# Optimization experiments

Measured on AMD Instinct MI355X. Metric: run time of the kernel, lower is better.

Reference implementation:

```python
import jax, jax.numpy as jnp
import numpy as np

NEG_INF = -1.0e9  # masked_fill value in the original


def gaussian_prior(n_heads, len_q, len_k, dtype=jnp.float32):
    """Per-head lower-triangular Gaussian positional bias.

    gm[h, i, j] = exp(-(j - i)^2 / (2 * sigma_h^2)) for i >= j, else 0.
    The buggy source never passes sigma_hs; we use sigma_h = h + 1 as a
    deterministic per-head bandwidth (wider Gaussians for later heads).
    """
    i = jnp.arange(len_q)[:, None]          # [Lq, 1]
    j = jnp.arange(len_k)[None, :]          # [1, Lk]
    d2 = (j - i).astype(dtype) ** 2         # [Lq, Lk]
    sigma = jnp.arange(1, n_heads + 1, dtype=dtype)  # [H]
    g = jnp.exp(-d2[None] / (2.0 * sigma[:, None, None] ** 2))  # [H, Lq, Lk]
    return jnp.where(i >= j, g, jnp.zeros((), dtype))[None]     # mask upper tri -> [1,H,Lq,Lk] via broadcast of where


def setup_inputs() -> dict:
    key = jax.random.key(0)
    kq, kk, kv = jax.random.split(key, 3)
    B, H, S, D = 2, 16, 2048, 128
    Q = jax.random.normal(kq, (B, H, S, D), dtype=jnp.float32)
    K = jax.random.normal(kk, (B, H, S, D), dtype=jnp.float32)
    V = jax.random.normal(kv, (B, H, S, D), dtype=jnp.float32)
    # Causal mask: True where attention is disallowed (j > i), broadcastable.
    i = jnp.arange(S)[:, None]
    j = jnp.arange(S)[None, :]
    attn_mask = (j > i)[None, None]  # [1,1,S,S] bool
    return {"Q": Q, "K": K, "V": V, "attn_mask": attn_mask}


def reference(Q, K, V, attn_mask):
    B, H, Lq, D = Q.shape
    Lk = K.shape[2]
    scale = 1.0 / np.sqrt(D).astype(np.float32)
    # scores: [B,H,Lq,Lk]
    scores = jnp.einsum("bhqd,bhkd->bhqk", Q, K) * scale
    gm = gaussian_prior(H, Lq, Lk, dtype=scores.dtype)  # [H,Lq,Lk] broadcast over batch
    scores = scores + gm
    scores = jnp.where(attn_mask, jnp.asarray(NEG_INF, scores.dtype), scores)
    attn = jax.nn.softmax(scores, axis=-1)
    context = jnp.einsum("bhqk,bhkd->bhqd", attn, V)
    return (context, attn)
```

## Files before the change

kernel.cpp:

```cpp
#include <hip/hip_runtime.h>

typedef __attribute__((ext_vector_type(8))) short s16x8;
typedef __attribute__((ext_vector_type(4))) float f32x4;
typedef __attribute__((ext_vector_type(16))) float f32x16;
typedef __attribute__((ext_vector_type(4))) int i32x4;


static __device__ __forceinline__ unsigned short f2bf(float f) {
  unsigned int u = __float_as_uint(f);
  u += 0x7fffu + ((u >> 16) & 1u);
  return (unsigned short)(u >> 16);
}

static __device__ __forceinline__ unsigned short* swz(unsigned short* base, int row,
                                                      int shift, int byte_in_row) {
  int b = (row << shift) + (byte_in_row ^ ((row & 7) << 4));
  return (unsigned short*)((char*)base + b);
}

static __device__ __forceinline__ s16x8 pack8(float4 a, float4 b) {
  s16x8 p;
  p[0] = (short)f2bf(a.x); p[1] = (short)f2bf(a.y);
  p[2] = (short)f2bf(a.z); p[3] = (short)f2bf(a.w);
  p[4] = (short)f2bf(b.x); p[5] = (short)f2bf(b.y);
  p[6] = (short)f2bf(b.z); p[7] = (short)f2bf(b.w);
  return p;
}

static __device__ __forceinline__ int cvtpk(float a, float b) {
  int r;
  asm("v_cvt_pk_bf16_f32 %0, %1, %2" : "=v"(r) : "v"(a), "v"(b));
  return r;
}

static __device__ __forceinline__ void plswap(int& x, int& y) {
  asm("v_permlane32_swap_b32 %0, %1" : "+v"(x), "+v"(y));
}

#define GLDS(gp, lp) __builtin_amdgcn_global_load_lds(                        \
    (const __attribute__((address_space(1))) void*)(gp),                      \
    (__attribute__((address_space(3))) void*)(lp), 16, 0, 0)

#define STAGE(ldsbase, gtile) do {                                            \
    const char* _g = (const char*)(gtile) + (w << 12) + (lane << 4);          \
    char* _l = (char*)(ldsbase) + (w << 12);                                  \
    GLDS(_g,        _l);                                                      \
    GLDS(_g + 1024, _l + 1024);                                               \
    GLDS(_g + 2048, _l + 2048);                                               \
    GLDS(_g + 3072, _l + 3072);                                               \
  } while (0)


__global__ void pack_kv(const float* __restrict__ Kg, const float* __restrict__ Vg,
                        unsigned short* __restrict__ Kw, unsigned short* __restrict__ Vw) {
  __shared__ float Vs[8192];
  const int blk = (int)blockIdx.x;
  const float* Kb = Kg + ((size_t)blk << 13);
  const float* Vb = Vg + ((size_t)blk << 13);
  unsigned short* Ko = Kw + ((size_t)blk << 13);
  unsigned short* Vo = Vw + ((size_t)blk << 13);
  int c = (int)threadIdx.x;
  #pragma unroll
  for (int it = 0; it < 4; ++it, c += 256) {
    int r = c >> 4, c8 = (c & 15) << 3;
    int dst = r * 128 + ((((c8 << 1)) ^ ((r & 7) << 4)) >> 1);
    const float4* s4 = (const float4*)(Kb + r * 128 + c8);
    *(s16x8*)(Ko + dst) = pack8(s4[0], s4[1]);
  }
  c = (int)threadIdx.x;
  #pragma unroll
  for (int it = 0; it < 8; ++it, c += 256)
    *(float4*)(Vs + (c << 2)) = *(const float4*)(Vb + (c << 2));
  __syncthreads();
  c = (int)threadIdx.x;
  #pragma unroll
  for (int it = 0; it < 4; ++it, c += 256) {
    int d = c & 127, j0 = (c >> 7) << 3;
    s16x8 p;
    #pragma unroll
    for (int e = 0; e < 8; ++e) p[e] = (short)f2bf(Vs[(j0 + e) * 128 + d]);
    int dst = d * 64 + ((((j0 << 1)) ^ ((d & 7) << 4)) >> 1);
    *(s16x8*)(Vo + dst) = p;
  }
}


__global__ __launch_bounds__(256, 2)
void gpsdpa4(const float* __restrict__ Qg, const unsigned short* __restrict__ Kw,
             const unsigned short* __restrict__ Vw, float* __restrict__ Og,
             float* __restrict__ Ag) {
  __shared__ alignas(16) unsigned short KV[4][8192];
  __shared__ float red[128];

  const int tid  = (int)threadIdx.x;
  const int w    = tid >> 6;
  const int lane = tid & 63;
  const int l31  = lane & 31;
  const int hi   = lane >> 5;
  const int qh   = w >> 1;
  const int jh   = w & 1;

  const int bh = (int)blockIdx.x & 31;
  const int qt = 31 - ((int)blockIdx.x >> 5);
  const int h  = bh & 15;
  const int q0 = qt << 6;

  const float* Qb = Qg + ((size_t)bh << 18) + ((size_t)q0 << 7);
  const unsigned short* Kb = Kw + ((size_t)(bh << 5) << 13);
  const unsigned short* Vb = Vw + ((size_t)(bh << 5) << 13);
  float* Ob = Og + ((size_t)bh << 18) + ((size_t)q0 << 7);
  float* Ab = Ag + ((size_t)bh << 22);

  const float sig = (float)(h + 1);
  const float cst = -1.0f / (2.0f * sig * sig);
  const float scale = 0.08838834764831845f;

  s16x8 bQ[8];
  {
    const float* qr = Qb + ((qh << 5) + l31) * 128 + (hi << 3);
    #pragma unroll
    for (int dk = 0; dk < 8; ++dk) {
      const float4* s4 = (const float4*)(qr + (dk << 4));
      bQ[dk] = pack8(s4[0], s4[1]);
    }
  }

  const int iq   = q0 + (qh << 5) + l31;
  const int krow = (jh << 5) + l31;
  const int kswz = (krow & 7) << 4;

  float psum = 0.f;
  const int nst = (qt >> 1) + 1;
  STAGE(&KV[0][0], Kb);
  STAGE(&KV[1][0], Kb + ((size_t)1 << 13));
  for (int s = 0; s < nst; ++s) {
    const int cur = s & 1;
    __syncthreads();
    if (s + 1 < nst) {
      STAGE(&KV[(cur ^ 1) << 1][0],       Kb + ((size_t)(2 * s + 2) << 13));
      STAGE(&KV[((cur ^ 1) << 1) + 1][0], Kb + ((size_t)(2 * s + 3) << 13));
    }
    #pragma unroll
    for (int half = 0; half < 2; ++half) {
      const int t = 2 * s + half;
      if (t > qt) break;
      if ((t == qt) && (jh > qh)) continue;
      const char* KtC = (const char*)&KV[(cur << 1) + half][0] + krow * 256;

      f32x16 acc = (f32x16)0.0f;
      #pragma unroll
      for (int dk = 0; dk < 8; ++dk) {
        s16x8 aK = *(const s16x8*)(KtC + (((dk << 5) + (hi << 4)) ^ kswz));
        acc = __builtin_amdgcn_mfma_f32_32x32x16_bf16(aK, bQ[dk], acc, 0, 0, 0);
      }

      if (t <= qt - 3) {
        #pragma unroll
        for (int r = 0; r < 16; ++r)
          psum += __expf(fmaf(acc[r], scale, -8.0f));
      } else if (t < qt || jh < qh) {
        #pragma unroll
        for (int r = 0; r < 16; ++r) {
          int j = (t << 6) + (jh << 5) + (r & 3) + ((r >> 2) << 3) + (hi << 2);
          float fd = (float)(iq - j);
          psum += __expf(fmaf(acc[r], scale, __expf(fd * fd * cst) - 8.0f));
        }
      } else {
        #pragma unroll
        for (int r = 0; r < 16; ++r) {
          int j = (t << 6) + (jh << 5) + (r & 3) + ((r >> 2) << 3) + (hi << 2);
          int dist = iq - j;
          float fd = (float)dist;
          float x = fmaf(acc[r], scale, __expf(fd * fd * cst) - 8.0f);
          psum += (dist >= 0) ? __expf(x) : 0.f;
        }
      }
    }
  }

  psum += __shfl_xor(psum, 32, 64);
  __syncthreads();
  if (lane < 32) red[(((qh << 1) | jh) << 5) + l31] = psum;
  __syncthreads();
  const float tot = psum + red[(((qh << 1) | (jh ^ 1)) << 5) + l31];
  const float lrs = -8.0f - __logf(tot);

  f32x16 oacc[4];
  #pragma unroll
  for (int dn = 0; dn < 4; ++dn) oacc[dn] = (f32x16)0.0f;

  __syncthreads();
  STAGE(&KV[0][0], Kb);
  STAGE(&KV[2][0], Vb);

  for (int t = 0; t <= qt; ++t) {
    const int cur = t & 1;
    __syncthreads();
    if (t < qt) {
      STAGE(&KV[cur ^ 1][0],       Kb + ((size_t)(t + 1) << 13));
      STAGE(&KV[2 + (cur ^ 1)][0], Vb + ((size_t)(t + 1) << 13));
    }

    const bool skipq = (t == qt) && (jh > qh);
    float p[16];
    if (!skipq) {
      const char* KtC = (const char*)&KV[cur][0] + krow * 256;
      f32x16 acc = (f32x16)0.0f;
      #pragma unroll
      for (int dk = 0; dk < 8; ++dk) {
        s16x8 aK = *(const s16x8*)(KtC + (((dk << 5) + (hi << 4)) ^ kswz));
        acc = __builtin_amdgcn_mfma_f32_32x32x16_bf16(aK, bQ[dk], acc, 0, 0, 0);
      }
      if (t <= qt - 3) {
        #pragma unroll
        for (int r = 0; r < 16; ++r)
          p[r] = __expf(fmaf(acc[r], scale, lrs));
      } else if (t < qt || jh < qh) {
        #pragma unroll
        for (int r = 0; r < 16; ++r) {
          int j = (t << 6) + (jh << 5) + (r & 3) + ((r >> 2) << 3) + (hi << 2);
          float fd = (float)(iq - j);
          p[r] = __expf(fmaf(acc[r], scale, __expf(fd * fd * cst) + lrs));
        }
      } else {
        #pragma unroll
        for (int r = 0; r < 16; ++r) {
          int j = (t << 6) + (jh << 5) + (r & 3) + ((r >> 2) << 3) + (hi << 2);
          int dist = iq - j;
          float fd = (float)dist;
          float x = fmaf(acc[r], scale, __expf(fd * fd * cst) + lrs);
          p[r] = (dist >= 0) ? __expf(x) : 0.f;
        }
      }
    } else {
      #pragma unroll
      for (int r = 0; r < 16; ++r) p[r] = 0.f;
    }

    {
      float* arow = Ab + (size_t)iq * 2048 + (t << 6) + (jh << 5) + (hi << 2);
      *(float4*)(arow)      = make_float4(p[0],  p[1],  p[2],  p[3]);
      *(float4*)(arow + 8)  = make_float4(p[4],  p[5],  p[6],  p[7]);
      *(float4*)(arow + 16) = make_float4(p[8],  p[9],  p[10], p[11]);
      *(float4*)(arow + 24) = make_float4(p[12], p[13], p[14], p[15]);
    }

    if (!skipq) {
      const char* VtC = (const char*)&KV[2 + cur][0];
      #pragma unroll
      for (int ks = 0; ks < 2; ++ks) {
        int x0 = cvtpk(p[8 * ks + 0], p[8 * ks + 1]);
        int x1 = cvtpk(p[8 * ks + 2], p[8 * ks + 3]);
        int y0 = cvtpk(p[8 * ks + 4], p[8 * ks + 5]);
        int y1 = cvtpk(p[8 * ks + 6], p[8 * ks + 7]);
        plswap(x0, y0);
        plswap(x1, y1);
        i32x4 pk4; pk4[0] = x0; pk4[1] = x1; pk4[2] = y0; pk4[3] = y1;
        s16x8 pa = *(s16x8*)&pk4;
        #pragma unroll
        for (int dn = 0; dn < 4; ++dn) {
          int vrow = (dn << 5) + l31;
          s16x8 vb = *(const s16x8*)((const char*)VtC + vrow * 128 +
                       (((jh << 6) + (ks << 5) + (hi << 4)) ^ ((vrow & 7) << 4)));
          oacc[dn] = __builtin_amdgcn_mfma_f32_32x32x16_bf16(pa, vb, oacc[dn], 0, 0, 0);
        }
      }
    }
  }

  __syncthreads();
  float* cts = (float*)&KV[0][0];
  if (jh == 1) {
    #pragma unroll
    for (int dn = 0; dn < 4; ++dn)
      #pragma unroll
      for (int r = 0; r < 16; ++r) {
        int qrow = (r & 3) + ((r >> 2) << 3) + (hi << 2);
        cts[(qh << 12) + qrow * 128 + (dn << 5) + l31] = oacc[dn][r];
      }
  }
  __syncthreads();
  if (jh == 0) {
    #pragma unroll
    for (int dn = 0; dn < 4; ++dn)
      #pragma unroll
      for (int r = 0; r < 16; ++r) {
        int qrow = (r & 3) + ((r >> 2) << 3) + (hi << 2);
        float v = oacc[dn][r] + cts[(qh << 12) + qrow * 128 + (dn << 5) + l31];
        Ob[(size_t)((qh << 5) + qrow) * 128 + (dn << 5) + l31] = v;
      }
  }

  const float4 z4 = make_float4(0.f, 0.f, 0.f, 0.f);
  for (int tt = qt + 1; tt < 32; ++tt) {
    float4* dst = (float4*)(Ab + (size_t)q0 * 2048 + (tt << 6));
    int f = tid;
    #pragma unroll
    for (int k = 0; k < 4; ++k, f += 256) {
      int r = f >> 4, cc = f & 15;
      dst[(size_t)r * 512 + cc] = z4;
    }
  }
}


__global__ __launch_bounds__(256, 2)
void gpsdpa_fb(const float* __restrict__ Qg, const float* __restrict__ Kg,
               const float* __restrict__ Vg, float* __restrict__ Og,
               float* __restrict__ Ag) {
  __shared__ alignas(16) unsigned short Qs[64 * 128];
  __shared__ alignas(16) unsigned short Ksl[64 * 128];
  __shared__ alignas(16) unsigned short Vtl[128 * 64];
  __shared__ alignas(16) unsigned short Ps[4][16 * 64];
  __shared__ float gtab[2048];

  const int tid  = (int)threadIdx.x;
  const int w    = tid >> 6;
  const int lane = tid & 63;
  const int l15  = lane & 15;
  const int g    = lane >> 4;

  const int bh = (int)blockIdx.x & 31;
  const int qt = 31 - ((int)blockIdx.x >> 5);
  const int h  = bh & 15;
  const int q0 = qt << 6;

  const size_t base = (size_t)bh << 18;
  const float* Qb = Qg + base + (size_t)q0 * 128;
  const float* Kb = Kg + base;
  const float* Vb = Vg + base;
  float* Ob = Og + base;
  float* Ab = Ag + ((size_t)bh << 22);

  {
    float sig = (float)(h + 1);
    float c = -1.0f / (2.0f * sig * sig);
    for (int d = tid; d < 2048; d += 256) {
      float fd = (float)d;
      gtab[d] = __expf(fd * fd * c);
    }
  }

  {
    int c = tid;
    #pragma unroll
    for (int it = 0; it < 4; ++it, c += 256) {
      int r = c >> 4, c8 = (c & 15) << 3;
      const float4* s4 = (const float4*)(Qb + (size_t)r * 128 + c8);
      *(s16x8*)swz(Qs, r, 8, c8 * 2) = pack8(s4[0], s4[1]);
    }
  }
  __syncthreads();

  s16x8 aQ[4];
  #pragma unroll
  for (int kc = 0; kc < 4; ++kc)
    aQ[kc] = *(const s16x8*)swz(Qs, (w << 4) + l15, 8, (kc << 6) + (g << 4));

  const float scale = 0.08838834764831845f;
  const int ibase = q0 + (w << 4) + (g << 2);

  float m_r[4], ls_r[4];
  #pragma unroll
  for (int r = 0; r < 4; ++r) { m_r[r] = -3.0e38f; ls_r[r] = 0.0f; }

  const f32x4 fzero = {0.f, 0.f, 0.f, 0.f};

  for (int t = 0; t <= qt; ++t) {
    __syncthreads();
    {
      int c = tid;
      #pragma unroll
      for (int it = 0; it < 4; ++it, c += 256) {
        int r = c >> 4, c8 = (c & 15) << 3;
        const float4* s4 = (const float4*)(Kb + (size_t)((t << 6) + r) * 128 + c8);
        *(s16x8*)swz(Ksl, r, 8, c8 * 2) = pack8(s4[0], s4[1]);
      }
    }
    __syncthreads();

    f32x4 acc[4];
    #pragma unroll
    for (int n = 0; n < 4; ++n) acc[n] = fzero;
    #pragma unroll
    for (int kc = 0; kc < 4; ++kc) {
      #pragma unroll
      for (int n = 0; n < 4; ++n) {
        s16x8 bK = *(const s16x8*)swz(Ksl, (n << 4) + l15, 8, (kc << 6) + (g << 4));
        acc[n] = __builtin_amdgcn_mfma_f32_16x16x32_bf16(aQ[kc], bK, acc[n], 0, 0, 0);
      }
    }

    const int jb = (t << 6) + l15;
    #pragma unroll
    for (int r = 0; r < 4; ++r) {
      const int i = ibase + r;
      float sv[4];
      float mx = -3.0e38f;
      #pragma unroll
      for (int n = 0; n < 4; ++n) {
        int dist = i - (jb + (n << 4));
        float x = (dist >= 0) ? (acc[n][r] * scale + gtab[dist]) : -1.0e9f;
        sv[n] = x;
        mx = fmaxf(mx, x);
      }
      #pragma unroll
      for (int mk = 1; mk < 16; mk <<= 1) mx = fmaxf(mx, __shfl_xor(mx, mk, 64));
      float mn = fmaxf(m_r[r], mx);
      float sm = 0.f;
      #pragma unroll
      for (int n = 0; n < 4; ++n) sm += __expf(sv[n] - mn);
      #pragma unroll
      for (int mk = 1; mk < 16; mk <<= 1) sm += __shfl_xor(sm, mk, 64);
      ls_r[r] = ls_r[r] * __expf(m_r[r] - mn) + sm;
      m_r[r] = mn;
    }
  }

  float rls[4];
  #pragma unroll
  for (int r = 0; r < 4; ++r) rls[r] = 1.0f / ls_r[r];

  f32x4 oacc[8];
  #pragma unroll
  for (int dn = 0; dn < 8; ++dn) oacc[dn] = fzero;

  unsigned short* Pw = &Ps[w][0];

  for (int t = 0; t <= qt; ++t) {
    __syncthreads();
    {
      int c = tid;
      #pragma unroll
      for (int it = 0; it < 4; ++it, c += 256) {
        int r = c >> 4, c8 = (c & 15) << 3;
        const float4* s4 = (const float4*)(Kb + (size_t)((t << 6) + r) * 128 + c8);
        *(s16x8*)swz(Ksl, r, 8, c8 * 2) = pack8(s4[0], s4[1]);
      }
      c = tid;
      #pragma unroll
      for (int it = 0; it < 4; ++it, c += 256) {
        int d = c & 127, j0 = (c >> 7) << 3;
        const float* vs = Vb + (size_t)((t << 6) + j0) * 128 + d;
        s16x8 p;
        #pragma unroll
        for (int e = 0; e < 8; ++e) p[e] = (short)f2bf(vs[(size_t)e * 128]);
        *(s16x8*)swz(Vtl, d, 7, j0 * 2) = p;
      }
    }
    __syncthreads();

    f32x4 acc[4];
    #pragma unroll
    for (int n = 0; n < 4; ++n) acc[n] = fzero;
    #pragma unroll
    for (int kc = 0; kc < 4; ++kc) {
      #pragma unroll
      for (int n = 0; n < 4; ++n) {
        s16x8 bK = *(const s16x8*)swz(Ksl, (n << 4) + l15, 8, (kc << 6) + (g << 4));
        acc[n] = __builtin_amdgcn_mfma_f32_16x16x32_bf16(aQ[kc], bK, acc[n], 0, 0, 0);
      }
    }

    const int jb = (t << 6) + l15;
    #pragma unroll
    for (int r = 0; r < 4; ++r) {
      const int i = ibase + r;
      float* arow = Ab + (size_t)i * 2048 + (t << 6) + l15;
      #pragma unroll
      for (int n = 0; n < 4; ++n) {
        int dist = i - (jb + (n << 4));
        float x = (dist >= 0) ? (acc[n][r] * scale + gtab[dist]) : -1.0e9f;
        float p = __expf(x - m_r[r]) * rls[r];
        arow[n << 4] = p;
        *swz(Pw, (g << 2) + r, 7, ((n << 4) + l15) << 1) = f2bf(p);
      }
    }

    #pragma unroll
    for (int kc2 = 0; kc2 < 2; ++kc2) {
      s16x8 pa = *(const s16x8*)swz(Pw, l15, 7, (kc2 << 6) + (g << 4));
      #pragma unroll
      for (int dn = 0; dn < 8; ++dn) {
        s16x8 vb = *(const s16x8*)swz(Vtl, (dn << 4) + l15, 7, (kc2 << 6) + (g << 4));
        oacc[dn] = __builtin_amdgcn_mfma_f32_16x16x32_bf16(pa, vb, oacc[dn], 0, 0, 0);
      }
    }
  }

  #pragma unroll
  for (int dn = 0; dn < 8; ++dn) {
    #pragma unroll
    for (int r = 0; r < 4; ++r) {
      Ob[(size_t)(ibase + r) * 128 + (dn << 4) + l15] = oacc[dn][r];
    }
  }

  const int jmax = (qt + 1) << 6;
  if (jmax < 2048) {
    for (int r = 0; r < 64; ++r) {
      float4* dst = (float4*)(Ab + (size_t)(q0 + r) * 2048);
      for (int cv = (jmax >> 2) + tid; cv < 512; cv += 256) {
        dst[cv] = make_float4(0.f, 0.f, 0.f, 0.f);
      }
    }
  }
}


extern "C" void kernel_launch(void* const* d_in, const int* in_sizes, int n_in,
                              void* d_out, int out_size, void* d_ws, size_t ws_size,
                              hipStream_t stream) {
  (void)in_sizes; (void)n_in; (void)out_size;
  const float* Q = (const float*)d_in[0];
  const float* K = (const float*)d_in[1];
  const float* V = (const float*)d_in[2];
  float* ctx  = (float*)d_out;
  float* attn = ctx + (size_t)2 * 16 * 2048 * 128;
  dim3 grid(1024), block(256);

  const size_t NEED = (size_t)2 << 24;
  if (ws_size >= NEED) {
    unsigned short* Kw = (unsigned short*)d_ws;
    unsigned short* Vw = Kw + ((size_t)1 << 23);
    pack_kv<<<grid, block, 0, stream>>>(K, V, Kw, Vw);
    gpsdpa4<<<grid, block, 0, stream>>>(Q, Kw, Vw, ctx, attn);
  } else {
    gpsdpa_fb<<<grid, block, 0, stream>>>(Q, K, V, ctx, attn);
  }
}
```

Measured before the change: 220.2 us.

## Use exp2 with folded log2e, raise MFMA priority, relax barriers with explicit vmcnt waits

Folds log2(e) into the scale, the Gaussian constant and the offset so the softmax exponentials map directly onto the hardware exp2 instruction. Wraps the MFMA sequences in s_setprio to favour matrix issue across waves. Replaces the per-iteration __syncthreads in the second pass with a raw s_barrier plus manual vmcnt waits, so outstanding global stores of the attention matrix need not drain before each barrier. The manual waitcnt scheme is fragile: it depends on how STAGE issues its loads and on the count of stores in flight, and a wrong count could race on LDS.

```diff
diff --git a/kernel.cpp b/kernel.cpp
--- a/kernel.cpp
+++ b/kernel.cpp
@@ -86,7 +86,7 @@
 
 
 __global__ __launch_bounds__(256, 2)
-void gpsdpa4(const float* __restrict__ Qg, const unsigned short* __restrict__ Kw,
+void gpsdpa5(const float* __restrict__ Qg, const unsigned short* __restrict__ Kw,
              const unsigned short* __restrict__ Vw, float* __restrict__ Og,
              float* __restrict__ Ag) {
   __shared__ alignas(16) unsigned short KV[4][8192];
@@ -111,9 +111,11 @@
   float* Ob = Og + ((size_t)bh << 18) + ((size_t)q0 << 7);
   float* Ab = Ag + ((size_t)bh << 22);
 
+  const float L2E = 1.4426950408889634f;
   const float sig = (float)(h + 1);
-  const float cst = -1.0f / (2.0f * sig * sig);
-  const float scale = 0.08838834764831845f;
+  const float cst2 = (-1.0f / (2.0f * sig * sig)) * L2E;
+  const float scale2 = 0.08838834764831845f * L2E;
+  const float B1 = -11.541560327111707f;
 
   s16x8 bQ[8];
   {
@@ -148,22 +150,25 @@
       const char* KtC = (const char*)&KV[(cur << 1) + half][0] + krow * 256;
 
       f32x16 acc = (f32x16)0.0f;
+      __builtin_amdgcn_s_setprio(1);
       #pragma unroll
       for (int dk = 0; dk < 8; ++dk) {
         s16x8 aK = *(const s16x8*)(KtC + (((dk << 5) + (hi << 4)) ^ kswz));
         acc = __builtin_amdgcn_mfma_f32_32x32x16_bf16(aK, bQ[dk], acc, 0, 0, 0);
       }
+      __builtin_amdgcn_s_setprio(0);
 
       if (t <= qt - 3) {
         #pragma unroll
         for (int r = 0; r < 16; ++r)
-          psum += __expf(fmaf(acc[r], scale, -8.0f));
+          psum += __builtin_amdgcn_exp2f(fmaf(acc[r], scale2, B1));
       } else if (t < qt || jh < qh) {
         #pragma unroll
         for (int r = 0; r < 16; ++r) {
           int j = (t << 6) + (jh << 5) + (r & 3) + ((r >> 2) << 3) + (hi << 2);
           float fd = (float)(iq - j);
-          psum += __expf(fmaf(acc[r], scale, __expf(fd * fd * cst) - 8.0f));
+          float g = __builtin_amdgcn_exp2f(fd * fd * cst2);
+          psum += __builtin_amdgcn_exp2f(fmaf(acc[r], scale2, fmaf(g, L2E, B1)));
         }
       } else {
         #pragma unroll
@@ -171,8 +176,9 @@
           int j = (t << 6) + (jh << 5) + (r & 3) + ((r >> 2) << 3) + (hi << 2);
           int dist = iq - j;
           float fd = (float)dist;
-          float x = fmaf(acc[r], scale, __expf(fd * fd * cst) - 8.0f);
-          psum += (dist >= 0) ? __expf(x) : 0.f;
+          float g = __builtin_amdgcn_exp2f(fd * fd * cst2);
+          float x = __builtin_amdgcn_exp2f(fmaf(acc[r], scale2, fmaf(g, L2E, B1)));
+          psum += (dist >= 0) ? x : 0.f;
         }
       }
     }
@@ -183,19 +189,20 @@
   if (lane < 32) red[(((qh << 1) | jh) << 5) + l31] = psum;
   __syncthreads();
   const float tot = psum + red[(((qh << 1) | (jh ^ 1)) << 5) + l31];
-  const float lrs = -8.0f - __logf(tot);
+  const float lrs2 = B1 - __log2f(tot);
 
   f32x16 oacc[4];
   #pragma unroll
   for (int dn = 0; dn < 4; ++dn) oacc[dn] = (f32x16)0.0f;
 
-  __syncthreads();
   STAGE(&KV[0][0], Kb);
   STAGE(&KV[2][0], Vb);
+  asm volatile("s_waitcnt vmcnt(0)" ::: "memory");
 
   for (int t = 0; t <= qt; ++t) {
     const int cur = t & 1;
-    __syncthreads();
+    __builtin_amdgcn_s_barrier();
+    __builtin_amdgcn_sched_barrier(0);
     if (t < qt) {
       STAGE(&KV[cur ^ 1][0],       Kb + ((size_t)(t + 1) << 13));
       STAGE(&KV[2 + (cur ^ 1)][0], Vb + ((size_t)(t + 1) << 13));
@@ -206,21 +213,24 @@
     if (!skipq) {
       const char* KtC = (const char*)&KV[cur][0] + krow * 256;
       f32x16 acc = (f32x16)0.0f;
+      __builtin_amdgcn_s_setprio(1);
       #pragma unroll
       for (int dk = 0; dk < 8; ++dk) {
         s16x8 aK = *(const s16x8*)(KtC + (((dk << 5) + (hi << 4)) ^ kswz));
         acc = __builtin_amdgcn_mfma_f32_32x32x16_bf16(aK, bQ[dk], acc, 0, 0, 0);
       }
+      __builtin_amdgcn_s_setprio(0);
       if (t <= qt - 3) {
         #pragma unroll
         for (int r = 0; r < 16; ++r)
-          p[r] = __expf(fmaf(acc[r], scale, lrs));
+          p[r] = __builtin_amdgcn_exp2f(fmaf(acc[r], scale2, lrs2));
       } else if (t < qt || jh < qh) {
         #pragma unroll
         for (int r = 0; r < 16; ++r) {
           int j = (t << 6) + (jh << 5) + (r & 3) + ((r >> 2) << 3) + (hi << 2);
           float fd = (float)(iq - j);
-          p[r] = __expf(fmaf(acc[r], scale, __expf(fd * fd * cst) + lrs));
+          float g = __builtin_amdgcn_exp2f(fd * fd * cst2);
+          p[r] = __builtin_amdgcn_exp2f(fmaf(acc[r], scale2, fmaf(g, L2E, lrs2)));
         }
       } else {
         #pragma unroll
@@ -228,8 +238,9 @@
           int j = (t << 6) + (jh << 5) + (r & 3) + ((r >> 2) << 3) + (hi << 2);
           int dist = iq - j;
           float fd = (float)dist;
-          float x = fmaf(acc[r], scale, __expf(fd * fd * cst) + lrs);
-          p[r] = (dist >= 0) ? __expf(x) : 0.f;
+          float g = __builtin_amdgcn_exp2f(fd * fd * cst2);
+          float x = __builtin_amdgcn_exp2f(fmaf(acc[r], scale2, fmaf(g, L2E, lrs2)));
+          p[r] = (dist >= 0) ? x : 0.f;
         }
       }
     } else {
@@ -257,6 +268,7 @@
         plswap(x1, y1);
         i32x4 pk4; pk4[0] = x0; pk4[1] = x1; pk4[2] = y0; pk4[3] = y1;
         s16x8 pa = *(s16x8*)&pk4;
+        __builtin_amdgcn_s_setprio(1);
         #pragma unroll
         for (int dn = 0; dn < 4; ++dn) {
           int vrow = (dn << 5) + l31;
@@ -264,8 +276,11 @@
                        (((jh << 6) + (ks << 5) + (hi << 4)) ^ ((vrow & 7) << 4)));
           oacc[dn] = __builtin_amdgcn_mfma_f32_32x32x16_bf16(pa, vb, oacc[dn], 0, 0, 0);
         }
-      }
-    }
+        __builtin_amdgcn_s_setprio(0);
+      }
+    }
+
+    asm volatile("s_waitcnt vmcnt(4)" ::: "memory");
   }
 
   __syncthreads();
@@ -524,7 +539,7 @@
     unsigned short* Kw = (unsigned short*)d_ws;
     unsigned short* Vw = Kw + ((size_t)1 << 23);
     pack_kv<<<grid, block, 0, stream>>>(K, V, Kw, Vw);
-    gpsdpa4<<<grid, block, 0, stream>>>(Q, Kw, Vw, ctx, attn);
+    gpsdpa5<<<grid, block, 0, stream>>>(Q, Kw, Vw, ctx, attn);
   } else {
     gpsdpa_fb<<<grid, block, 0, stream>>>(Q, K, V, ctx, attn);
   }
```

Result: slower. 226.2 us (+2.7%).
